# Optimization experiments

Hardware: AMD Instinct MI355X
Metric: run time of the kernel (lower is better)

The kernel has to match this reference:

```python
import jax, jax.numpy as jnp
import numpy as np

E = 8          # num experts
TOPK = 2
D = 1024       # emb_size (expert hidden == emb_size)


def setup_inputs() -> dict:
    key = jax.random.key(0)
    ks = jax.random.split(key, 8)
    s = 1.0 / np.sqrt(D)
    x = jax.random.normal(ks[0], (4, 1024, D), dtype=jnp.float32)
    gate_W = jax.random.uniform(ks[1], (E, D), jnp.float32, -s, s)   # torch Linear weight (out,in)
    gate_b = jax.random.uniform(ks[2], (E,), jnp.float32, -s, s)
    w1 = jax.random.uniform(ks[3], (E, D, D), jnp.float32, -s, s)    # per-expert first Linear (out,in)
    b1 = jax.random.uniform(ks[4], (E, D), jnp.float32, -s, s)
    w2 = jax.random.uniform(ks[5], (E, D, D), jnp.float32, -s, s)    # per-expert second Linear (out,in)
    b2 = jax.random.uniform(ks[6], (E, D), jnp.float32, -s, s)
    return {"x": x, "gate_W": gate_W, "gate_b": gate_b,
            "w1": w1, "b1": b1, "w2": w2, "b2": b2}


def reference(x, gate_W, gate_b, w1, b1, w2, b2):
    x_shape = x.shape
    xt = x.reshape(-1, x_shape[-1])                       # [N, D]

    # gating
    gate_logits = xt @ gate_W.T + gate_b                  # [N, E]
    gate_prob = jax.nn.softmax(gate_logits, axis=-1)      # [N, E]
    top_w, top_i = jax.lax.top_k(gate_prob, TOPK)         # [N, K]
    top_w = jax.nn.softmax(top_w, axis=-1)                # renormalize over top-k

    # dense per-expert MLP: h = relu(x @ W1^T + b1); o = h @ W2^T + b2
    h = jax.nn.relu(jnp.einsum('nd,ehd->neh', xt, w1) + b1[None])   # [N, E, D]
    o = jnp.einsum('neh,eoh->neo', h, w2) + b2[None]                # [N, E, D]

    # gather top-k expert outputs per token and combine with weights
    o_top = jnp.take_along_axis(o, top_i[:, :, None], axis=1)       # [N, K, D]
    y = jnp.sum(o_top * top_w[:, :, None], axis=1)                  # [N, D]

    return y.reshape(x_shape), gate_prob
```

## Files before the change

kernel.cpp:

```cpp
#include <hip/hip_runtime.h>

#define NTOK 4096
#define DIM 1024
#define NE 8
#define NPAIR (NTOK * 2)

typedef __bf16 bf16x8 __attribute__((ext_vector_type(8)));
typedef float floatx4 __attribute__((ext_vector_type(4)));

__device__ __forceinline__ unsigned short f2bf(float f) {
  unsigned u = __float_as_uint(f);
  u = u + 0x7fffu + ((u >> 16) & 1u);
  return (unsigned short)(u >> 16);
}
__device__ __forceinline__ float bf2f(unsigned short h) {
  return __uint_as_float(((unsigned)h) << 16);
}

__device__ __forceinline__ void gld_lds16(const unsigned short* g, unsigned short* l) {
  __builtin_amdgcn_global_load_lds(
      (const __attribute__((address_space(1))) void*)g,
      (__attribute__((address_space(3))) void*)l, 16, 0, 0);
}

__global__ __launch_bounds__(256) void gate_kernel(
    const float* __restrict__ x, const float* __restrict__ gW,
    const float* __restrict__ gb,
    float* __restrict__ gp_out, int2* __restrict__ tops,
    float* __restrict__ pairw, int* __restrict__ cnt, int* __restrict__ done)
{
  const int tid = threadIdx.x;
  if (blockIdx.x == 0) {
    if (tid < NE) cnt[tid] = 0;
    if (tid == NE) *done = 0;
  }
  const int lane = tid & 63;
  const int wid = tid >> 6;
  const int t = blockIdx.x * 4 + wid;

  float4 xv[4];
#pragma unroll
  for (int j = 0; j < 4; j++)
    xv[j] = ((const float4*)(x + (size_t)t * DIM))[lane + 64 * j];

  float p[NE];
#pragma unroll
  for (int e = 0; e < NE; e++) {
    const float4* gwe = (const float4*)(gW + e * DIM);
    float s = 0.f;
#pragma unroll
    for (int j = 0; j < 4; j++) {
      float4 g = gwe[lane + 64 * j];
      s += xv[j].x * g.x + xv[j].y * g.y + xv[j].z * g.z + xv[j].w * g.w;
    }
    p[e] = s;
  }
#pragma unroll
  for (int e = 0; e < NE; e++) {
#pragma unroll
    for (int off = 32; off >= 1; off >>= 1) p[e] += __shfl_xor(p[e], off);
  }

  float m = -1e30f;
#pragma unroll
  for (int e = 0; e < NE; e++) { p[e] += gb[e]; m = fmaxf(m, p[e]); }
  float s = 0.f;
  float pr[NE];
#pragma unroll
  for (int e = 0; e < NE; e++) { pr[e] = __expf(p[e] - m); s += pr[e]; }
  float inv = 1.f / s;
#pragma unroll
  for (int e = 0; e < NE; e++) pr[e] *= inv;

  if (lane < NE) gp_out[(size_t)t * NE + lane] = pr[lane];

  if (lane == 0) {
    int i0 = 0;
#pragma unroll
    for (int e = 1; e < NE; e++) if (pr[e] > pr[i0]) i0 = e;
    int i1 = (i0 == 0) ? 1 : 0;
#pragma unroll
    for (int e = 0; e < NE; e++) if (e != i0 && pr[e] > pr[i1]) i1 = e;
    float d = __expf(pr[i1] - pr[i0]);
    float w0 = 1.f / (1.f + d);
    tops[t] = make_int2(i0, i1);
    pairw[t * 2] = w0;
    pairw[t * 2 + 1] = 1.f - w0;
  }
}

__global__ __launch_bounds__(256) void bin_sched_kernel(
    const int2* __restrict__ tops, int* __restrict__ cnt,
    int* __restrict__ bucket,
    int* __restrict__ posmap,
    int* __restrict__ done, int* __restrict__ base,
    int* __restrict__ sched, int* __restrict__ sched_n)
{
  const int t = blockIdx.x * 256 + threadIdx.x;
  const int lane = threadIdx.x & 63;
  int2 ti = tops[t];
#pragma unroll
  for (int slot = 0; slot < 2; slot++) {
    int e = slot ? ti.y : ti.x;
#pragma unroll
    for (int ex = 0; ex < NE; ex++) {
      bool mine = (e == ex);
      unsigned long long mask = __ballot(mine);
      if (mask) {
        int leader = __ffsll((long long)mask) - 1;
        int total = __popcll(mask);
        int prefix = __popcll(mask & ((1ull << lane) - 1ull));
        int idx = 0;
        if (lane == leader) idx = atomicAdd(&cnt[ex], total);
        idx = __shfl(idx, leader) + prefix;
        if (mine) {
          bucket[ex * NTOK + idx] = t * 2 + slot;
          posmap[t * 2 + slot] = (ex << 16) | idx;
        }
      }
    }
  }
  __syncthreads();
  if (threadIdx.x == 0) {
    if (atomicAdd(done, 1) == gridDim.x - 1) {
      int b = 0, pos = 0;
      for (int e = 0; e < NE; e++) {
        int c = atomicAdd(&cnt[e], 0);
        base[e] = b;
        int tiles = (c + 127) >> 7;
        for (int i = 0; i < tiles; i++) {
          int valid = c - i * 128; if (valid > 128) valid = 128;
          sched[pos++] = (e << 20) | (i << 8) | valid;
        }
        b += c;
      }
      base[NE] = b;
      *sched_n = pos;
    }
  }
}

__global__ __launch_bounds__(256) void cvt_kernel(
    const float4* __restrict__ src, ushort4* __restrict__ dst)
{
  const int i = blockIdx.x * 256 + threadIdx.x;
  float4 v = src[i];
  ushort4 o;
  o.x = f2bf(v.x); o.y = f2bf(v.y); o.z = f2bf(v.z); o.w = f2bf(v.w);
  dst[i] = o;
}

__global__ __launch_bounds__(256) void gather_kernel(
    const float* __restrict__ x, const int* __restrict__ bucket,
    const int* __restrict__ base, unsigned short* __restrict__ A_pack)
{
  const int p = blockIdx.x;
  int e = 0;
#pragma unroll
  for (int k = 0; k < NE - 1; k++) if (p >= base[k + 1]) e = k + 1;
  const int pair = bucket[e * NTOK + (p - base[e])];
  const int tok = pair >> 1;
  const int tid = threadIdx.x;
  float4 v = ((const float4*)(x + (size_t)tok * DIM))[tid];
  ushort4 o;
  o.x = f2bf(v.x); o.y = f2bf(v.y); o.z = f2bf(v.z); o.w = f2bf(v.w);
  ((ushort4*)(A_pack + (size_t)p * DIM))[tid] = o;
}

template <int RELU>
__global__ __launch_bounds__(256) void ffn_gemm(
    const unsigned short* __restrict__ A,
    const unsigned short* __restrict__ B,
    const float* __restrict__ bias,
    const int* __restrict__ base,
    const int* __restrict__ sched, const int* __restrict__ sched_n,
    unsigned short* __restrict__ Out)
{
  const int l = blockIdx.x;
  const int xcd = l & 7;
  const int w = l >> 3;
  const int nt = w & 7;
  const int slot = xcd * 9 + (w >> 3);
  if (slot >= *sched_n) return;
  const int se = sched[slot];
  const int e = se >> 20;
  const int mt = (se >> 8) & 0xfff;
  const int valid = se & 255;
  const int arow0 = base[e] + mt * 128;

  __shared__ unsigned short lda[128 * 64];
  __shared__ unsigned short ldb[128 * 64];

  const int tid = threadIdx.x;
  const int lane = tid & 63;
  const int wid = tid >> 6;

  const unsigned short* ap[4];
  const unsigned short* bp[4];
#pragma unroll
  for (int j = 0; j < 4; j++) {
    int g = wid * 4 + j;
    int row = g * 8 + (lane >> 3);
    int gran = (lane & 7) ^ (row & 7);
    int prow = arow0 + row;
    if (prow > NPAIR - 1) prow = NPAIR - 1;
    ap[j] = A + (size_t)prow * DIM + (gran << 3);
    bp[j] = B + ((size_t)e * DIM + nt * 128 + row) * DIM + (gran << 3);
  }

  floatx4 acc[4][4] = {};
  const int wm = (wid & 1) * 64;
  const int wn = (wid >> 1) * 64;
  const int quad = lane >> 4;
  const int cl = lane & 15;
  const int sw = cl & 7;

  for (int k0 = 0; k0 < 16; k0++) {
#pragma unroll
    for (int j = 0; j < 4; j++) {
      int g = wid * 4 + j;
      gld_lds16(ap[j], &lda[g * 512]);
      gld_lds16(bp[j], &ldb[g * 512]);
      ap[j] += 64;
      bp[j] += 64;
    }
    __syncthreads();
#pragma unroll
    for (int kk = 0; kk < 64; kk += 32) {
      const int gb = (kk >> 3) + quad;
      const int goff = ((gb ^ sw) << 3);
      bf16x8 af[4], bfr[4];
#pragma unroll
      for (int mi = 0; mi < 4; mi++)
        af[mi] = *(const bf16x8*)&lda[(wm + mi * 16 + cl) * 64 + goff];
#pragma unroll
      for (int ni = 0; ni < 4; ni++)
        bfr[ni] = *(const bf16x8*)&ldb[(wn + ni * 16 + cl) * 64 + goff];
#pragma unroll
      for (int mi = 0; mi < 4; mi++)
#pragma unroll
        for (int ni = 0; ni < 4; ni++)
          acc[mi][ni] = __builtin_amdgcn_mfma_f32_16x16x32_bf16(af[mi], bfr[ni], acc[mi][ni], 0, 0, 0);
    }
    if (k0 < 15) __syncthreads();
  }

#pragma unroll
  for (int ni = 0; ni < 4; ni++) {
    int col = nt * 128 + wn + ni * 16 + cl;
    float bval = bias[e * DIM + col];
#pragma unroll
    for (int mi = 0; mi < 4; mi++) {
#pragma unroll
      for (int reg = 0; reg < 4; reg++) {
        int rl = wm + mi * 16 + quad * 4 + reg;
        if (rl < valid) {
          float v = acc[mi][ni][reg] + bval;
          if (RELU) v = fmaxf(v, 0.f);
          Out[(size_t)(arow0 + rl) * DIM + col] = f2bf(v);
        }
      }
    }
  }
}

__global__ __launch_bounds__(256) void combine_kernel(
    const unsigned short* __restrict__ o, const int* __restrict__ posmap,
    const int* __restrict__ base, const float* __restrict__ pairw,
    float* __restrict__ y)
{
  const int t = blockIdx.x;
  const int tid = threadIdx.x;
  const int pm0 = posmap[t * 2], pm1 = posmap[t * 2 + 1];
  const int p0 = base[pm0 >> 16] + (pm0 & 0xffff);
  const int p1 = base[pm1 >> 16] + (pm1 & 0xffff);
  const float w0 = pairw[t * 2], w1 = pairw[t * 2 + 1];
  ushort4 a = ((const ushort4*)(o + (size_t)p0 * DIM))[tid];
  ushort4 b = ((const ushort4*)(o + (size_t)p1 * DIM))[tid];
  float4 r;
  r.x = w0 * bf2f(a.x) + w1 * bf2f(b.x);
  r.y = w0 * bf2f(a.y) + w1 * bf2f(b.y);
  r.z = w0 * bf2f(a.z) + w1 * bf2f(b.z);
  r.w = w0 * bf2f(a.w) + w1 * bf2f(b.w);
  ((float4*)(y + (size_t)t * DIM))[tid] = r;
}

extern "C" void kernel_launch(void* const* d_in, const int* in_sizes, int n_in,
                              void* d_out, int out_size, void* d_ws, size_t ws_size,
                              hipStream_t stream) {
  const float* x  = (const float*)d_in[0];
  const float* gW = (const float*)d_in[1];
  const float* gb = (const float*)d_in[2];
  const float* w1 = (const float*)d_in[3];
  const float* b1 = (const float*)d_in[4];
  const float* w2 = (const float*)d_in[5];
  const float* b2 = (const float*)d_in[6];
  float* y  = (float*)d_out;
  float* gp = (float*)d_out + (size_t)NTOK * DIM;

  char* ws = (char*)d_ws;
  unsigned short* A_pack = (unsigned short*)(ws);
  unsigned short* w2_bf  = (unsigned short*)(ws);
  unsigned short* h_pack = (unsigned short*)(ws + (size_t)(16u << 20));
  unsigned short* w1_bf  = (unsigned short*)(ws + (size_t)(32u << 20));
  unsigned short* o_pack = (unsigned short*)(ws + (size_t)(32u << 20));
  char* tail = ws + (size_t)(48u << 20);
  int*   cnt     = (int*)(tail);
  int*   done    = cnt + NE;
  int*   base    = done + 1;
  int*   sched   = base + NE + 1;
  int*   sched_n = sched + 128;
  int*   bucket  = sched_n + 1;
  float* pairw   = (float*)(bucket + NE * NTOK);
  int2*  tops    = (int2*)(pairw + NPAIR);
  int*   posmap  = (int*)(tops + NTOK);

  const int cvt_blocks = (NE * DIM * DIM / 4) / 256;
  gate_kernel<<<NTOK / 4, 256, 0, stream>>>(x, gW, gb, gp, tops, pairw, cnt, done);
  bin_sched_kernel<<<NTOK / 256, 256, 0, stream>>>(tops, cnt, bucket, posmap, done,
                                                   base, sched, sched_n);
  cvt_kernel<<<cvt_blocks, 256, 0, stream>>>((const float4*)w1, (ushort4*)w1_bf);
  gather_kernel<<<NPAIR, 256, 0, stream>>>(x, bucket, base, A_pack);
  ffn_gemm<1><<<576, 256, 0, stream>>>(A_pack, w1_bf, b1, base, sched, sched_n, h_pack);
  cvt_kernel<<<cvt_blocks, 256, 0, stream>>>((const float4*)w2, (ushort4*)w2_bf);
  ffn_gemm<0><<<576, 256, 0, stream>>>(h_pack, w2_bf, b2, base, sched, sched_n, o_pack);
  combine_kernel<<<NTOK, 256, 0, stream>>>(o_pack, posmap, base, pairw, y);
}
```

Measured before the change: 239.7 us.

## Fuse token gather into first GEMM and double-buffer LDS K-loop

The gate kernel now writes a bf16 copy of x, and the first FFN GEMM loads its A rows indirectly through the bucket indices. This removes the separate gather kernel and its packed copy. Both GEMMs now double-buffer LDS tiles, issuing the next K-slice's global-to-LDS loads before computing the current one, so memory latency overlaps with MFMA work. The cost is doubled LDS per block, which may lower occupancy, and scattered row reads in the first GEMM.

```diff
diff --git a/kernel.cpp b/kernel.cpp
--- a/kernel.cpp
+++ b/kernel.cpp
@@ -27,7 +27,8 @@
     const float* __restrict__ x, const float* __restrict__ gW,
     const float* __restrict__ gb,
     float* __restrict__ gp_out, int2* __restrict__ tops,
-    float* __restrict__ pairw, int* __restrict__ cnt, int* __restrict__ done)
+    float* __restrict__ pairw, int* __restrict__ cnt, int* __restrict__ done,
+    unsigned short* __restrict__ x_bf)
 {
   const int tid = threadIdx.x;
   if (blockIdx.x == 0) {
@@ -42,6 +43,14 @@
 #pragma unroll
   for (int j = 0; j < 4; j++)
     xv[j] = ((const float4*)(x + (size_t)t * DIM))[lane + 64 * j];
+
+#pragma unroll
+  for (int j = 0; j < 4; j++) {
+    ushort4 o;
+    o.x = f2bf(xv[j].x); o.y = f2bf(xv[j].y);
+    o.z = f2bf(xv[j].z); o.w = f2bf(xv[j].w);
+    ((ushort4*)(x_bf + (size_t)t * DIM))[lane + 64 * j] = o;
+  }
 
   float p[NE];
 #pragma unroll
@@ -150,29 +159,13 @@
   dst[i] = o;
 }
 
-__global__ __launch_bounds__(256) void gather_kernel(
-    const float* __restrict__ x, const int* __restrict__ bucket,
-    const int* __restrict__ base, unsigned short* __restrict__ A_pack)
-{
-  const int p = blockIdx.x;
-  int e = 0;
-#pragma unroll
-  for (int k = 0; k < NE - 1; k++) if (p >= base[k + 1]) e = k + 1;
-  const int pair = bucket[e * NTOK + (p - base[e])];
-  const int tok = pair >> 1;
-  const int tid = threadIdx.x;
-  float4 v = ((const float4*)(x + (size_t)tok * DIM))[tid];
-  ushort4 o;
-  o.x = f2bf(v.x); o.y = f2bf(v.y); o.z = f2bf(v.z); o.w = f2bf(v.w);
-  ((ushort4*)(A_pack + (size_t)p * DIM))[tid] = o;
-}
-
-template <int RELU>
+template <int RELU, int GATHER>
 __global__ __launch_bounds__(256) void ffn_gemm(
     const unsigned short* __restrict__ A,
     const unsigned short* __restrict__ B,
     const float* __restrict__ bias,
     const int* __restrict__ base,
+    const int* __restrict__ bucket,
     const int* __restrict__ sched, const int* __restrict__ sched_n,
     unsigned short* __restrict__ Out)
 {
@@ -188,8 +181,8 @@
   const int valid = se & 255;
   const int arow0 = base[e] + mt * 128;
 
-  __shared__ unsigned short lda[128 * 64];
-  __shared__ unsigned short ldb[128 * 64];
+  __shared__ unsigned short lda[2][128 * 64];
+  __shared__ unsigned short ldb[2][128 * 64];
 
   const int tid = threadIdx.x;
   const int lane = tid & 63;
@@ -202,9 +195,17 @@
     int g = wid * 4 + j;
     int row = g * 8 + (lane >> 3);
     int gran = (lane & 7) ^ (row & 7);
-    int prow = arow0 + row;
-    if (prow > NPAIR - 1) prow = NPAIR - 1;
-    ap[j] = A + (size_t)prow * DIM + (gran << 3);
+    if (GATHER) {
+      int idx = mt * 128 + row;
+      int ce = base[e + 1] - base[e];
+      if (idx > ce - 1) idx = ce - 1;
+      int tok = bucket[e * NTOK + idx] >> 1;
+      ap[j] = A + (size_t)tok * DIM + (gran << 3);
+    } else {
+      int prow = arow0 + row;
+      if (prow > NPAIR - 1) prow = NPAIR - 1;
+      ap[j] = A + (size_t)prow * DIM + (gran << 3);
+    }
     bp[j] = B + ((size_t)e * DIM + nt * 128 + row) * DIM + (gran << 3);
   }
 
@@ -215,16 +216,19 @@
   const int cl = lane & 15;
   const int sw = cl & 7;
 
-  for (int k0 = 0; k0 < 16; k0++) {
+  auto stage = [&](int b) {
 #pragma unroll
     for (int j = 0; j < 4; j++) {
       int g = wid * 4 + j;
-      gld_lds16(ap[j], &lda[g * 512]);
-      gld_lds16(bp[j], &ldb[g * 512]);
+      gld_lds16(ap[j], &lda[b][g * 512]);
+      gld_lds16(bp[j], &ldb[b][g * 512]);
       ap[j] += 64;
       bp[j] += 64;
     }
-    __syncthreads();
+  };
+  auto compute = [&](int b) {
+    const unsigned short* la = lda[b];
+    const unsigned short* lb = ldb[b];
 #pragma unroll
     for (int kk = 0; kk < 64; kk += 32) {
       const int gb = (kk >> 3) + quad;
@@ -232,18 +236,38 @@
       bf16x8 af[4], bfr[4];
 #pragma unroll
       for (int mi = 0; mi < 4; mi++)
-        af[mi] = *(const bf16x8*)&lda[(wm + mi * 16 + cl) * 64 + goff];
+        af[mi] = *(const bf16x8*)&la[(wm + mi * 16 + cl) * 64 + goff];
 #pragma unroll
       for (int ni = 0; ni < 4; ni++)
-        bfr[ni] = *(const bf16x8*)&ldb[(wn + ni * 16 + cl) * 64 + goff];
+        bfr[ni] = *(const bf16x8*)&lb[(wn + ni * 16 + cl) * 64 + goff];
 #pragma unroll
       for (int mi = 0; mi < 4; mi++)
 #pragma unroll
         for (int ni = 0; ni < 4; ni++)
           acc[mi][ni] = __builtin_amdgcn_mfma_f32_16x16x32_bf16(af[mi], bfr[ni], acc[mi][ni], 0, 0, 0);
     }
-    if (k0 < 15) __syncthreads();
-  }
+  };
+
+  stage(0);
+  asm volatile("s_waitcnt vmcnt(0)" ::: "memory");
+  __builtin_amdgcn_s_barrier();
+
+#pragma unroll 1
+  for (int i = 0; i < 7; i++) {
+    stage(1);
+    compute(0);
+    asm volatile("s_waitcnt vmcnt(0)" ::: "memory");
+    __builtin_amdgcn_s_barrier();
+    stage(0);
+    compute(1);
+    asm volatile("s_waitcnt vmcnt(0)" ::: "memory");
+    __builtin_amdgcn_s_barrier();
+  }
+  stage(1);
+  compute(0);
+  asm volatile("s_waitcnt vmcnt(0)" ::: "memory");
+  __builtin_amdgcn_s_barrier();
+  compute(1);
 
 #pragma unroll
   for (int ni = 0; ni < 4; ni++) {
@@ -299,7 +323,7 @@
   float* gp = (float*)d_out + (size_t)NTOK * DIM;
 
   char* ws = (char*)d_ws;
-  unsigned short* A_pack = (unsigned short*)(ws);
+  unsigned short* x_bf   = (unsigned short*)(ws);
   unsigned short* w2_bf  = (unsigned short*)(ws);
   unsigned short* h_pack = (unsigned short*)(ws + (size_t)(16u << 20));
   unsigned short* w1_bf  = (unsigned short*)(ws + (size_t)(32u << 20));
@@ -316,13 +340,12 @@
   int*   posmap  = (int*)(tops + NTOK);
 
   const int cvt_blocks = (NE * DIM * DIM / 4) / 256;
-  gate_kernel<<<NTOK / 4, 256, 0, stream>>>(x, gW, gb, gp, tops, pairw, cnt, done);
+  gate_kernel<<<NTOK / 4, 256, 0, stream>>>(x, gW, gb, gp, tops, pairw, cnt, done, x_bf);
   bin_sched_kernel<<<NTOK / 256, 256, 0, stream>>>(tops, cnt, bucket, posmap, done,
                                                    base, sched, sched_n);
   cvt_kernel<<<cvt_blocks, 256, 0, stream>>>((const float4*)w1, (ushort4*)w1_bf);
-  gather_kernel<<<NPAIR, 256, 0, stream>>>(x, bucket, base, A_pack);
-  ffn_gemm<1><<<576, 256, 0, stream>>>(A_pack, w1_bf, b1, base, sched, sched_n, h_pack);
+  ffn_gemm<1, 1><<<576, 256, 0, stream>>>(x_bf, w1_bf, b1, base, bucket, sched, sched_n, h_pack);
   cvt_kernel<<<cvt_blocks, 256, 0, stream>>>((const float4*)w2, (ushort4*)w2_bf);
-  ffn_gemm<0><<<576, 256, 0, stream>>>(h_pack, w2_bf, b2, base, sched, sched_n, o_pack);
+  ffn_gemm<0, 0><<<576, 256, 0, stream>>>(h_pack, w2_bf, b2, base, bucket, sched, sched_n, o_pack);
   combine_kernel<<<NTOK, 256, 0, stream>>>(o_pack, posmap, base, pairw, y);
 }
```

Result: slower. 264.0 us (+10.2%).
